# Performance work log

Hardware: AMD Instinct MI355X
Metric: run time of the kernel (lower is better)

## Reference

```python
import jax, jax.numpy as jnp
import numpy as np

ALPHA = 0.2  # LeakyReLU negative slope
NEG_INF = -9e15


def setup_inputs() -> dict:
    key = jax.random.key(0)
    ks = jax.random.split(key, 6)
    B, N, F_IN, F_OUT = 4, 1024, 64, 64
    h = jax.random.normal(ks[0], (B, N, F_IN), dtype=jnp.float32)
    adj = jax.random.randint(ks[1], (B, N, N), 0, 2, dtype=jnp.int32)
    lin_w = jax.random.normal(ks[2], (F_OUT, F_IN), dtype=jnp.float32) * (1.0 / np.sqrt(F_IN))
    lin_b = jax.random.normal(ks[3], (F_OUT,), dtype=jnp.float32) * 0.02
    W_w = jax.random.normal(ks[4], (F_OUT, 2 * F_OUT), dtype=jnp.float32) * (1.0 / np.sqrt(2 * F_OUT))
    a = jax.random.normal(ks[5], (F_OUT, 1), dtype=jnp.float32) * (1.414 / np.sqrt(F_OUT))
    return {"h": h, "adj": adj, "lin_w": lin_w, "lin_b": lin_b, "W_w": W_w, "a": a}


def reference(h, adj, lin_w, lin_b, W_w, a):
    F_OUT = lin_w.shape[0]
    # h' = Linear(h): (B, N, F_OUT)
    hp = jnp.einsum('bni,oi->bno', h, lin_w) + lin_b
    # W @ concat(h_i, h_j) == h_i @ W1^T + h_j @ W2^T  (same math, no 2F concat)
    W1, W2 = W_w[:, :F_OUT], W_w[:, F_OUT:]
    u = jnp.einsum('bnf,of->bno', hp, W1)  # source/row term   (B, N, F_OUT)
    v = jnp.einsum('bnf,of->bno', hp, W2)  # target/col term   (B, N, F_OUT)
    s = u[:, :, None, :] + v[:, None, :, :]        # (B, N, N, F_OUT)
    s = jnp.where(s > 0, s, ALPHA * s)             # LeakyReLU
    e = jnp.einsum('bijf,f->bij', s, a[:, 0])      # (B, N, N)
    e = jnp.where(adj > 0, e, NEG_INF)
    attention = jax.nn.softmax(e, axis=2)
    h_prime = jnp.einsum('bij,bjf->bif', attention, hp)
    return jax.nn.elu(h_prime)
```

## Files before the change

### kernel.cpp

```cpp
#include <hip/hip_runtime.h>
#include <hip/hip_bf16.h>
#include <math.h>

constexpr int B = 4;
constexpr int N = 1024;
constexpr float NEGINF = -9000000000000000.0f;

__global__ __launch_bounds__(512) void gat_wk0(
    const float* __restrict__ lin_w, const float* __restrict__ lin_b,
    const float* __restrict__ W_w, float* __restrict__ Wu, float* __restrict__ Wv,
    float* __restrict__ bu, float* __restrict__ bv) {
  __shared__ float lw[64 * 68];
  __shared__ float ww[64 * 132];
  __shared__ float lb[64];
  const int tid = threadIdx.x;
  for (int idx = tid; idx < 4096; idx += 512)
    lw[(idx >> 6) * 68 + (idx & 63)] = lin_w[idx];
  for (int idx = tid; idx < 8192; idx += 512)
    ww[(idx >> 7) * 132 + (idx & 127)] = W_w[idx];
  if (tid < 64) lb[tid] = lin_b[tid];
  __syncthreads();

  const int f = tid >> 3, i0 = (tid & 7) << 3;
  float wua[8], wva[8];
#pragma unroll
  for (int r = 0; r < 8; ++r) { wua[r] = 0.f; wva[r] = 0.f; }
  float bup = 0.f, bvp = 0.f;
#pragma unroll 4
  for (int o = 0; o < 64; ++o) {
    const float w1 = ww[f * 132 + o];
    const float w2 = ww[f * 132 + 64 + o];
    const float4 A = *(const float4*)&lw[o * 68 + i0];
    const float4 Bv = *(const float4*)&lw[o * 68 + i0 + 4];
    const float lv[8] = {A.x, A.y, A.z, A.w, Bv.x, Bv.y, Bv.z, Bv.w};
#pragma unroll
    for (int r = 0; r < 8; ++r) {
      wua[r] = fmaf(w1, lv[r], wua[r]);
      wva[r] = fmaf(w2, lv[r], wva[r]);
    }
    bup = fmaf(w1, lb[o], bup);
    bvp = fmaf(w2, lb[o], bvp);
  }
  *(float4*)&Wu[f * 64 + i0] = make_float4(wua[0], wua[1], wua[2], wua[3]);
  *(float4*)&Wu[f * 64 + i0 + 4] = make_float4(wua[4], wua[5], wua[6], wua[7]);
  *(float4*)&Wv[f * 64 + i0] = make_float4(wva[0], wva[1], wva[2], wva[3]);
  *(float4*)&Wv[f * 64 + i0 + 4] = make_float4(wva[4], wva[5], wva[6], wva[7]);
  if ((tid & 7) == 0) { bu[f] = bup; bv[f] = bvp; }
}

__global__ __launch_bounds__(256) void gat_prep(
    const float* __restrict__ h, const float* __restrict__ lin_w,
    const float* __restrict__ lin_b, const float* __restrict__ a_g,
    const float* __restrict__ Wu, const float* __restrict__ Wv,
    const float* __restrict__ bu_g, const float* __restrict__ bv_g,
    float* __restrict__ hp, float* __restrict__ u_out, float* __restrict__ vT,
    float* __restrict__ au_out, float* __restrict__ av_out) {
  __shared__ float hs[64 * 34];
  __shared__ float wl[64 * 68];
  __shared__ float wu[64 * 68];
  __shared__ float wv[64 * 68];
  __shared__ float vt_s[64 * 33];
  __shared__ float ared[2][32 * 17];
  __shared__ float lb_s[64], bu_s[64], bv_s[64], a_s[64];

  const int b = blockIdx.x >> 5;
  const int n0 = (blockIdx.x & 31) << 5;
  const int tid = threadIdx.x;

  for (int idx = tid; idx < 2048; idx += 256) {
    const int r = idx >> 6, c = idx & 63;
    hs[c * 34 + r] = h[((b << 10) + n0 + r) * 64 + c];
  }
  for (int idx = tid; idx < 4096; idx += 256) {
    const int r = idx >> 6, c = idx & 63;
    wl[c * 68 + r] = lin_w[idx];
    wu[c * 68 + r] = Wu[idx];
    wv[c * 68 + r] = Wv[idx];
  }
  if (tid < 64) {
    lb_s[tid] = lin_b[tid]; bu_s[tid] = bu_g[tid];
    bv_s[tid] = bv_g[tid];  a_s[tid] = a_g[tid];
  }
  __syncthreads();

  const int tf = tid & 15, tn = tid >> 4;
  float ahp[2][4], aU[2][4], aV[2][4];
#pragma unroll
  for (int q = 0; q < 2; ++q)
#pragma unroll
    for (int r = 0; r < 4; ++r) {
      ahp[q][r] = lb_s[tf * 4 + r];
      aU[q][r] = bu_s[tf * 4 + r];
      aV[q][r] = bv_s[tf * 4 + r];
    }
#pragma unroll 4
  for (int k = 0; k < 64; ++k) {
    const float2 h2 = *(const float2*)&hs[k * 34 + tn * 2];
    const float hv[2] = {h2.x, h2.y};
    const float4 l4 = *(const float4*)&wl[k * 68 + tf * 4];
    const float4 u4 = *(const float4*)&wu[k * 68 + tf * 4];
    const float4 v4 = *(const float4*)&wv[k * 68 + tf * 4];
    const float lv[4] = {l4.x, l4.y, l4.z, l4.w};
    const float uv[4] = {u4.x, u4.y, u4.z, u4.w};
    const float vv[4] = {v4.x, v4.y, v4.z, v4.w};
#pragma unroll
    for (int q = 0; q < 2; ++q)
#pragma unroll
      for (int r = 0; r < 4; ++r) {
        ahp[q][r] = fmaf(hv[q], lv[r], ahp[q][r]);
        aU[q][r] = fmaf(hv[q], uv[r], aU[q][r]);
        aV[q][r] = fmaf(hv[q], vv[r], aV[q][r]);
      }
  }
#pragma unroll
  for (int q = 0; q < 2; ++q) {
    const int row = (b << 10) + n0 + tn * 2 + q;
    *(float4*)&hp[row * 64 + tf * 4] =
        make_float4(ahp[q][0], ahp[q][1], ahp[q][2], ahp[q][3]);
    *(float4*)&u_out[row * 64 + tf * 4] =
        make_float4(aU[q][0], aU[q][1], aU[q][2], aU[q][3]);
  }
  float aup[2] = {0.f, 0.f}, avp[2] = {0.f, 0.f};
#pragma unroll
  for (int q = 0; q < 2; ++q)
#pragma unroll
    for (int r = 0; r < 4; ++r) {
      vt_s[(tf * 4 + r) * 33 + tn * 2 + q] = aV[q][r];
      aup[q] = fmaf(a_s[tf * 4 + r], aU[q][r], aup[q]);
      avp[q] = fmaf(a_s[tf * 4 + r], aV[q][r], avp[q]);
    }
#pragma unroll
  for (int q = 0; q < 2; ++q) {
    ared[0][(tn * 2 + q) * 17 + tf] = aup[q];
    ared[1][(tn * 2 + q) * 17 + tf] = avp[q];
  }
  __syncthreads();
  for (int idx = tid; idx < 2048; idx += 256) {
    const int f = idx >> 5, n = idx & 31;
    vT[(((b << 6) + f) << 10) + n0 + n] = vt_s[f * 33 + n];
  }
  if (tid < 64) {
    const int which = tid >> 5, row = tid & 31;
    float s2 = 0.f;
#pragma unroll
    for (int t = 0; t < 16; ++t) s2 += ared[which][row * 17 + t];
    if (which == 0) au_out[(b << 10) + n0 + row] = s2;
    else av_out[(b << 10) + n0 + row] = s2;
  }
}

__global__ __launch_bounds__(256) void gat_attn(
    const float* __restrict__ u_g, const float* __restrict__ vT,
    const float* __restrict__ hp, const int* __restrict__ adj,
    const float* __restrict__ a_g, const float* __restrict__ au_g,
    const float* __restrict__ av_g, float* __restrict__ out) {
  __shared__ float p_s[2 * 1024 * 4];
  __shared__ float u_s[64 * 8];
  __shared__ float a_s[64];
  __shared__ float au_s[8];
  __shared__ float wred[4 * 8];
  __shared__ float wsum[4 * 8];
  __shared__ float rinv_s[8];

  const int b = blockIdx.x >> 7;
  const int i0 = (blockIdx.x & 127) << 3;
  const int tid = threadIdx.x;
  const int lane = tid & 63, w = tid >> 6;

  if (tid < 64) a_s[tid] = a_g[tid];
  if (tid < 8) au_s[tid] = au_g[(b << 10) + i0 + tid];
  for (int idx = tid; idx < 512; idx += 256) {
    const int i = idx >> 6, f = idx & 63;
    u_s[f * 8 + i] = u_g[((b << 10) + i0 + i) * 64 + f];
  }
  __syncthreads();

  float e[8][4];
#pragma unroll
  for (int i = 0; i < 8; ++i)
#pragma unroll
    for (int k = 0; k < 4; ++k) e[i][k] = 0.f;

  const float* vb = vT + ((b << 6) << 10);
#pragma unroll 2
  for (int f = 0; f < 64; ++f) {
    const float af = a_s[f];
    float vv[4];
#pragma unroll
    for (int k = 0; k < 4; ++k) vv[k] = vb[(f << 10) + tid + (k << 8)];
    const float4 ua = *(const float4*)&u_s[f * 8];
    const float4 ub = *(const float4*)&u_s[f * 8 + 4];
    const float uu[8] = {ua.x, ua.y, ua.z, ua.w, ub.x, ub.y, ub.z, ub.w};
#pragma unroll
    for (int i = 0; i < 8; ++i)
#pragma unroll
      for (int k = 0; k < 4; ++k)
        e[i][k] = fmaf(af, fabsf(uu[i] + vv[k]), e[i][k]);
  }
  float avv[4];
#pragma unroll
  for (int k = 0; k < 4; ++k)
    avv[k] = 0.6f * av_g[(b << 10) + tid + (k << 8)];
  float au6[8];
#pragma unroll
  for (int i = 0; i < 8; ++i) au6[i] = 0.6f * au_s[i];
  const int* adjb = adj + ((((b << 10) + i0)) << 10) + tid;
#pragma unroll
  for (int i = 0; i < 8; ++i)
#pragma unroll
    for (int k = 0; k < 4; ++k) {
      const float ev = fmaf(0.4f, e[i][k], au6[i] + avv[k]);
      e[i][k] = adjb[(i << 10) + (k << 8)] > 0 ? ev : NEGINF;
    }

#pragma unroll
  for (int i = 0; i < 8; ++i) {
    float mm = fmaxf(fmaxf(e[i][0], e[i][1]), fmaxf(e[i][2], e[i][3]));
#pragma unroll
    for (int off = 32; off; off >>= 1) mm = fmaxf(mm, __shfl_xor(mm, off));
    if (lane == 0) wred[w * 8 + i] = mm;
  }
  __syncthreads();
#pragma unroll
  for (int i = 0; i < 8; ++i) {
    const float mi = fmaxf(fmaxf(wred[i], wred[8 + i]),
                           fmaxf(wred[16 + i], wred[24 + i]));
#pragma unroll
    for (int k = 0; k < 4; ++k) e[i][k] = __expf(e[i][k] - mi);
    float ss = e[i][0] + e[i][1] + e[i][2] + e[i][3];
#pragma unroll
    for (int off = 32; off; off >>= 1) ss += __shfl_xor(ss, off);
    if (lane == 0) wsum[w * 8 + i] = ss;
  }
  __syncthreads();
#pragma unroll
  for (int i = 0; i < 8; ++i) {
    const float stot = wsum[i] + wsum[8 + i] + wsum[16 + i] + wsum[24 + i];
    if (tid == i) rinv_s[i] = 1.0f / stot;
  }
#pragma unroll
  for (int k = 0; k < 4; ++k) {
    const int j = tid + (k << 8);
    *(float4*)&p_s[j << 2] = make_float4(e[0][k], e[1][k], e[2][k], e[3][k]);
    *(float4*)&p_s[4096 + (j << 2)] =
        make_float4(e[4][k], e[5][k], e[6][k], e[7][k]);
  }
  __syncthreads();

  const int fl = tid & 63, g = tid >> 6;
  float acc[8];
#pragma unroll
  for (int i = 0; i < 8; ++i) acc[i] = 0.f;
  const float* hpb = hp + (b << 16);
#pragma unroll 4
  for (int jj = g << 8; jj < (g << 8) + 256; ++jj) {
    const float hv = hpb[(jj << 6) + fl];
    const float4 p0 = *(const float4*)&p_s[jj << 2];
    const float4 p1 = *(const float4*)&p_s[4096 + (jj << 2)];
    acc[0] = fmaf(p0.x, hv, acc[0]);
    acc[1] = fmaf(p0.y, hv, acc[1]);
    acc[2] = fmaf(p0.z, hv, acc[2]);
    acc[3] = fmaf(p0.w, hv, acc[3]);
    acc[4] = fmaf(p1.x, hv, acc[4]);
    acc[5] = fmaf(p1.y, hv, acc[5]);
    acc[6] = fmaf(p1.z, hv, acc[6]);
    acc[7] = fmaf(p1.w, hv, acc[7]);
  }
  __syncthreads();
  float* red = p_s;
#pragma unroll
  for (int i = 0; i < 8; ++i) red[((g << 3) + i) << 6 | fl] = acc[i];
  __syncthreads();
#pragma unroll
  for (int o = 0; o < 2; ++o) {
    const int idx = tid + (o << 8);
    const int i = idx >> 6, f = idx & 63;
    float r = red[(i << 6) + f] + red[((8 + i) << 6) + f] +
              red[((16 + i) << 6) + f] + red[((24 + i) << 6) + f];
    r *= rinv_s[i];
    out[((b << 10) + i0 + i) * 64 + f] = r > 0.f ? r : expm1f(r);
  }
}

extern "C" void kernel_launch(void* const* d_in, const int* in_sizes, int n_in,
                              void* d_out, int out_size, void* d_ws, size_t ws_size,
                              hipStream_t stream) {
  const float* h = (const float*)d_in[0];
  const int* adj = (const int*)d_in[1];
  const float* lin_w = (const float*)d_in[2];
  const float* lin_b = (const float*)d_in[3];
  const float* W_w = (const float*)d_in[4];
  const float* a = (const float*)d_in[5];
  float* outp = (float*)d_out;

  float* ws = (float*)d_ws;
  float* hp = ws;
  float* u = ws + 262144;
  float* vT = ws + 524288;
  float* au = ws + 786432;
  float* av = ws + 790528;
  float* Wu = ws + 794624;
  float* Wv = ws + 798720;
  float* bu = ws + 802816;
  float* bv = ws + 802880;

  gat_wk0<<<dim3(1), dim3(512), 0, stream>>>(lin_w, lin_b, W_w, Wu, Wv, bu, bv);
  gat_prep<<<dim3(128), dim3(256), 0, stream>>>(h, lin_w, lin_b, a, Wu, Wv, bu,
                                                bv, hp, u, vT, au, av);
  gat_attn<<<dim3(512), dim3(256), 0, stream>>>(u, vT, hp, adj, a, au, av, outp);
}
```

Measured before the change: 135.6 us.

## Drop weight-fold kernel and halve attention rows per block with vectorized loads

Removes the single-block gat_wk0 launch that pre-multiplied W1/W2 by lin_w. gat_prep now computes hp first, stages it transposed in shared memory, and applies W1/W2 in a second pass. The attention kernel now handles 4 rows per block instead of 8, doubling the grid to 1024 blocks. It also gives each thread 4 contiguous columns so vT, av and adj can be read with float4/int4 loads. The extra blocks recompute the vT loads more often and add more duplicated reads of hp, in exchange for more parallelism, one fewer launch and wider memory accesses.

```diff
diff --git a/kernel.cpp b/kernel.cpp
--- a/kernel.cpp
+++ b/kernel.cpp
@@ -6,62 +6,20 @@
 constexpr int N = 1024;
 constexpr float NEGINF = -9000000000000000.0f;
 
-__global__ __launch_bounds__(512) void gat_wk0(
-    const float* __restrict__ lin_w, const float* __restrict__ lin_b,
-    const float* __restrict__ W_w, float* __restrict__ Wu, float* __restrict__ Wv,
-    float* __restrict__ bu, float* __restrict__ bv) {
-  __shared__ float lw[64 * 68];
-  __shared__ float ww[64 * 132];
-  __shared__ float lb[64];
-  const int tid = threadIdx.x;
-  for (int idx = tid; idx < 4096; idx += 512)
-    lw[(idx >> 6) * 68 + (idx & 63)] = lin_w[idx];
-  for (int idx = tid; idx < 8192; idx += 512)
-    ww[(idx >> 7) * 132 + (idx & 127)] = W_w[idx];
-  if (tid < 64) lb[tid] = lin_b[tid];
-  __syncthreads();
-
-  const int f = tid >> 3, i0 = (tid & 7) << 3;
-  float wua[8], wva[8];
-#pragma unroll
-  for (int r = 0; r < 8; ++r) { wua[r] = 0.f; wva[r] = 0.f; }
-  float bup = 0.f, bvp = 0.f;
-#pragma unroll 4
-  for (int o = 0; o < 64; ++o) {
-    const float w1 = ww[f * 132 + o];
-    const float w2 = ww[f * 132 + 64 + o];
-    const float4 A = *(const float4*)&lw[o * 68 + i0];
-    const float4 Bv = *(const float4*)&lw[o * 68 + i0 + 4];
-    const float lv[8] = {A.x, A.y, A.z, A.w, Bv.x, Bv.y, Bv.z, Bv.w};
-#pragma unroll
-    for (int r = 0; r < 8; ++r) {
-      wua[r] = fmaf(w1, lv[r], wua[r]);
-      wva[r] = fmaf(w2, lv[r], wva[r]);
-    }
-    bup = fmaf(w1, lb[o], bup);
-    bvp = fmaf(w2, lb[o], bvp);
-  }
-  *(float4*)&Wu[f * 64 + i0] = make_float4(wua[0], wua[1], wua[2], wua[3]);
-  *(float4*)&Wu[f * 64 + i0 + 4] = make_float4(wua[4], wua[5], wua[6], wua[7]);
-  *(float4*)&Wv[f * 64 + i0] = make_float4(wva[0], wva[1], wva[2], wva[3]);
-  *(float4*)&Wv[f * 64 + i0 + 4] = make_float4(wva[4], wva[5], wva[6], wva[7]);
-  if ((tid & 7) == 0) { bu[f] = bup; bv[f] = bvp; }
-}
-
 __global__ __launch_bounds__(256) void gat_prep(
     const float* __restrict__ h, const float* __restrict__ lin_w,
-    const float* __restrict__ lin_b, const float* __restrict__ a_g,
-    const float* __restrict__ Wu, const float* __restrict__ Wv,
-    const float* __restrict__ bu_g, const float* __restrict__ bv_g,
+    const float* __restrict__ lin_b, const float* __restrict__ W_w,
+    const float* __restrict__ a_g,
     float* __restrict__ hp, float* __restrict__ u_out, float* __restrict__ vT,
     float* __restrict__ au_out, float* __restrict__ av_out) {
   __shared__ float hs[64 * 34];
   __shared__ float wl[64 * 68];
-  __shared__ float wu[64 * 68];
-  __shared__ float wv[64 * 68];
+  __shared__ float w1[64 * 68];
+  __shared__ float w2[64 * 68];
+  __shared__ float hpT[64 * 34];
   __shared__ float vt_s[64 * 33];
   __shared__ float ared[2][32 * 17];
-  __shared__ float lb_s[64], bu_s[64], bv_s[64], a_s[64];
+  __shared__ float lb_s[64], a_s[64];
 
   const int b = blockIdx.x >> 5;
   const int n0 = (blockIdx.x & 31) << 5;
@@ -72,51 +30,61 @@
     hs[c * 34 + r] = h[((b << 10) + n0 + r) * 64 + c];
   }
   for (int idx = tid; idx < 4096; idx += 256) {
-    const int r = idx >> 6, c = idx & 63;
-    wl[c * 68 + r] = lin_w[idx];
-    wu[c * 68 + r] = Wu[idx];
-    wv[c * 68 + r] = Wv[idx];
-  }
-  if (tid < 64) {
-    lb_s[tid] = lin_b[tid]; bu_s[tid] = bu_g[tid];
-    bv_s[tid] = bv_g[tid];  a_s[tid] = a_g[tid];
-  }
+    const int o = idx >> 6, f = idx & 63;
+    wl[f * 68 + o] = lin_w[idx];
+    w1[f * 68 + o] = W_w[o * 128 + f];
+    w2[f * 68 + o] = W_w[o * 128 + 64 + f];
+  }
+  if (tid < 64) { lb_s[tid] = lin_b[tid]; a_s[tid] = a_g[tid]; }
   __syncthreads();
 
   const int tf = tid & 15, tn = tid >> 4;
-  float ahp[2][4], aU[2][4], aV[2][4];
+  float ahp[2][4];
 #pragma unroll
   for (int q = 0; q < 2; ++q)
 #pragma unroll
-    for (int r = 0; r < 4; ++r) {
-      ahp[q][r] = lb_s[tf * 4 + r];
-      aU[q][r] = bu_s[tf * 4 + r];
-      aV[q][r] = bv_s[tf * 4 + r];
-    }
+    for (int r = 0; r < 4; ++r) ahp[q][r] = lb_s[tf * 4 + r];
 #pragma unroll 4
   for (int k = 0; k < 64; ++k) {
     const float2 h2 = *(const float2*)&hs[k * 34 + tn * 2];
+    const float4 l4 = *(const float4*)&wl[k * 68 + tf * 4];
     const float hv[2] = {h2.x, h2.y};
-    const float4 l4 = *(const float4*)&wl[k * 68 + tf * 4];
-    const float4 u4 = *(const float4*)&wu[k * 68 + tf * 4];
-    const float4 v4 = *(const float4*)&wv[k * 68 + tf * 4];
     const float lv[4] = {l4.x, l4.y, l4.z, l4.w};
-    const float uv[4] = {u4.x, u4.y, u4.z, u4.w};
-    const float vv[4] = {v4.x, v4.y, v4.z, v4.w};
 #pragma unroll
     for (int q = 0; q < 2; ++q)
 #pragma unroll
-      for (int r = 0; r < 4; ++r) {
-        ahp[q][r] = fmaf(hv[q], lv[r], ahp[q][r]);
-        aU[q][r] = fmaf(hv[q], uv[r], aU[q][r]);
-        aV[q][r] = fmaf(hv[q], vv[r], aV[q][r]);
-      }
+      for (int r = 0; r < 4; ++r) ahp[q][r] = fmaf(hv[q], lv[r], ahp[q][r]);
   }
 #pragma unroll
   for (int q = 0; q < 2; ++q) {
     const int row = (b << 10) + n0 + tn * 2 + q;
     *(float4*)&hp[row * 64 + tf * 4] =
         make_float4(ahp[q][0], ahp[q][1], ahp[q][2], ahp[q][3]);
+#pragma unroll
+    for (int r = 0; r < 4; ++r) hpT[(tf * 4 + r) * 34 + tn * 2 + q] = ahp[q][r];
+  }
+  __syncthreads();
+
+  float aU[2][4] = {}, aV[2][4] = {};
+#pragma unroll 4
+  for (int k = 0; k < 64; ++k) {
+    const float2 h2 = *(const float2*)&hpT[k * 34 + tn * 2];
+    const float4 u4 = *(const float4*)&w1[k * 68 + tf * 4];
+    const float4 v4 = *(const float4*)&w2[k * 68 + tf * 4];
+    const float hv[2] = {h2.x, h2.y};
+    const float uv[4] = {u4.x, u4.y, u4.z, u4.w};
+    const float vv[4] = {v4.x, v4.y, v4.z, v4.w};
+#pragma unroll
+    for (int q = 0; q < 2; ++q)
+#pragma unroll
+      for (int r = 0; r < 4; ++r) {
+        aU[q][r] = fmaf(hv[q], uv[r], aU[q][r]);
+        aV[q][r] = fmaf(hv[q], vv[r], aV[q][r]);
+      }
+  }
+#pragma unroll
+  for (int q = 0; q < 2; ++q) {
+    const int row = (b << 10) + n0 + tn * 2 + q;
     *(float4*)&u_out[row * 64 + tf * 4] =
         make_float4(aU[q][0], aU[q][1], aU[q][2], aU[q][3]);
   }
@@ -154,129 +122,117 @@
     const float* __restrict__ hp, const int* __restrict__ adj,
     const float* __restrict__ a_g, const float* __restrict__ au_g,
     const float* __restrict__ av_g, float* __restrict__ out) {
-  __shared__ float p_s[2 * 1024 * 4];
-  __shared__ float u_s[64 * 8];
+  __shared__ float p_s[4 * 1024];
+  __shared__ float u_s[64 * 4];
   __shared__ float a_s[64];
-  __shared__ float au_s[8];
-  __shared__ float wred[4 * 8];
-  __shared__ float wsum[4 * 8];
-  __shared__ float rinv_s[8];
-
-  const int b = blockIdx.x >> 7;
-  const int i0 = (blockIdx.x & 127) << 3;
+  __shared__ float au_s[4];
+  __shared__ float wred[4][4];
+  __shared__ float wsum[4][4];
+  __shared__ float rinv_s[4];
+
+  const int b = blockIdx.x >> 8;
+  const int i0 = (blockIdx.x & 255) << 2;
   const int tid = threadIdx.x;
   const int lane = tid & 63, w = tid >> 6;
+  const int j0 = tid << 2;
 
   if (tid < 64) a_s[tid] = a_g[tid];
-  if (tid < 8) au_s[tid] = au_g[(b << 10) + i0 + tid];
-  for (int idx = tid; idx < 512; idx += 256) {
-    const int i = idx >> 6, f = idx & 63;
-    u_s[f * 8 + i] = u_g[((b << 10) + i0 + i) * 64 + f];
-  }
-  __syncthreads();
-
-  float e[8][4];
-#pragma unroll
-  for (int i = 0; i < 8; ++i)
+  if (tid < 4) au_s[tid] = au_g[(b << 10) + i0 + tid];
+  {
+    const int i = tid >> 6, f = tid & 63;
+    u_s[f * 4 + i] = u_g[((b << 10) + i0 + i) * 64 + f];
+  }
+  __syncthreads();
+
+  float e[4][4];
+#pragma unroll
+  for (int i = 0; i < 4; ++i)
 #pragma unroll
     for (int k = 0; k < 4; ++k) e[i][k] = 0.f;
 
   const float* vb = vT + ((b << 6) << 10);
-#pragma unroll 2
+#pragma unroll 4
   for (int f = 0; f < 64; ++f) {
     const float af = a_s[f];
-    float vv[4];
-#pragma unroll
-    for (int k = 0; k < 4; ++k) vv[k] = vb[(f << 10) + tid + (k << 8)];
-    const float4 ua = *(const float4*)&u_s[f * 8];
-    const float4 ub = *(const float4*)&u_s[f * 8 + 4];
-    const float uu[8] = {ua.x, ua.y, ua.z, ua.w, ub.x, ub.y, ub.z, ub.w};
-#pragma unroll
-    for (int i = 0; i < 8; ++i)
+    const float4 v4 = *(const float4*)&vb[(f << 10) + j0];
+    const float4 u4 = *(const float4*)&u_s[f * 4];
+    const float uu[4] = {u4.x, u4.y, u4.z, u4.w};
+    const float vv[4] = {v4.x, v4.y, v4.z, v4.w};
+#pragma unroll
+    for (int i = 0; i < 4; ++i)
 #pragma unroll
       for (int k = 0; k < 4; ++k)
         e[i][k] = fmaf(af, fabsf(uu[i] + vv[k]), e[i][k]);
   }
-  float avv[4];
-#pragma unroll
-  for (int k = 0; k < 4; ++k)
-    avv[k] = 0.6f * av_g[(b << 10) + tid + (k << 8)];
-  float au6[8];
-#pragma unroll
-  for (int i = 0; i < 8; ++i) au6[i] = 0.6f * au_s[i];
-  const int* adjb = adj + ((((b << 10) + i0)) << 10) + tid;
-#pragma unroll
-  for (int i = 0; i < 8; ++i)
+  const float4 av4 = *(const float4*)&av_g[(b << 10) + j0];
+  const float avv[4] = {0.6f * av4.x, 0.6f * av4.y, 0.6f * av4.z, 0.6f * av4.w};
+  float au6[4];
+#pragma unroll
+  for (int i = 0; i < 4; ++i) au6[i] = 0.6f * au_s[i];
+  const int* adjb = adj + ((((b << 10) + i0)) << 10) + j0;
+#pragma unroll
+  for (int i = 0; i < 4; ++i) {
+    const int4 ad = *(const int4*)&adjb[i << 10];
+    const int adv[4] = {ad.x, ad.y, ad.z, ad.w};
 #pragma unroll
     for (int k = 0; k < 4; ++k) {
       const float ev = fmaf(0.4f, e[i][k], au6[i] + avv[k]);
-      e[i][k] = adjb[(i << 10) + (k << 8)] > 0 ? ev : NEGINF;
+      e[i][k] = adv[k] > 0 ? ev : NEGINF;
     }
-
-#pragma unroll
-  for (int i = 0; i < 8; ++i) {
+  }
+
+#pragma unroll
+  for (int i = 0; i < 4; ++i) {
     float mm = fmaxf(fmaxf(e[i][0], e[i][1]), fmaxf(e[i][2], e[i][3]));
 #pragma unroll
     for (int off = 32; off; off >>= 1) mm = fmaxf(mm, __shfl_xor(mm, off));
-    if (lane == 0) wred[w * 8 + i] = mm;
-  }
-  __syncthreads();
-#pragma unroll
-  for (int i = 0; i < 8; ++i) {
-    const float mi = fmaxf(fmaxf(wred[i], wred[8 + i]),
-                           fmaxf(wred[16 + i], wred[24 + i]));
+    if (lane == 0) wred[w][i] = mm;
+  }
+  __syncthreads();
+#pragma unroll
+  for (int i = 0; i < 4; ++i) {
+    const float mi = fmaxf(fmaxf(wred[0][i], wred[1][i]),
+                           fmaxf(wred[2][i], wred[3][i]));
 #pragma unroll
     for (int k = 0; k < 4; ++k) e[i][k] = __expf(e[i][k] - mi);
     float ss = e[i][0] + e[i][1] + e[i][2] + e[i][3];
 #pragma unroll
     for (int off = 32; off; off >>= 1) ss += __shfl_xor(ss, off);
-    if (lane == 0) wsum[w * 8 + i] = ss;
-  }
-  __syncthreads();
-#pragma unroll
-  for (int i = 0; i < 8; ++i) {
-    const float stot = wsum[i] + wsum[8 + i] + wsum[16 + i] + wsum[24 + i];
-    if (tid == i) rinv_s[i] = 1.0f / stot;
-  }
-#pragma unroll
-  for (int k = 0; k < 4; ++k) {
-    const int j = tid + (k << 8);
-    *(float4*)&p_s[j << 2] = make_float4(e[0][k], e[1][k], e[2][k], e[3][k]);
-    *(float4*)&p_s[4096 + (j << 2)] =
-        make_float4(e[4][k], e[5][k], e[6][k], e[7][k]);
-  }
+    if (lane == 0) wsum[w][i] = ss;
+  }
+  __syncthreads();
+  if (tid < 4)
+    rinv_s[tid] = 1.0f / (wsum[0][tid] + wsum[1][tid] + wsum[2][tid] + wsum[3][tid]);
+#pragma unroll
+  for (int i = 0; i < 4; ++i)
+    *(float4*)&p_s[(i << 10) + j0] = make_float4(e[i][0], e[i][1], e[i][2], e[i][3]);
   __syncthreads();
 
   const int fl = tid & 63, g = tid >> 6;
-  float acc[8];
-#pragma unroll
-  for (int i = 0; i < 8; ++i) acc[i] = 0.f;
+  float acc[4] = {0.f, 0.f, 0.f, 0.f};
   const float* hpb = hp + (b << 16);
-#pragma unroll 4
-  for (int jj = g << 8; jj < (g << 8) + 256; ++jj) {
-    const float hv = hpb[(jj << 6) + fl];
-    const float4 p0 = *(const float4*)&p_s[jj << 2];
-    const float4 p1 = *(const float4*)&p_s[4096 + (jj << 2)];
-    acc[0] = fmaf(p0.x, hv, acc[0]);
-    acc[1] = fmaf(p0.y, hv, acc[1]);
-    acc[2] = fmaf(p0.z, hv, acc[2]);
-    acc[3] = fmaf(p0.w, hv, acc[3]);
-    acc[4] = fmaf(p1.x, hv, acc[4]);
-    acc[5] = fmaf(p1.y, hv, acc[5]);
-    acc[6] = fmaf(p1.z, hv, acc[6]);
-    acc[7] = fmaf(p1.w, hv, acc[7]);
+  for (int jj = g << 8; jj < (g << 8) + 256; jj += 4) {
+    const float4 p0 = *(const float4*)&p_s[jj];
+    const float4 p1 = *(const float4*)&p_s[1024 + jj];
+    const float4 p2 = *(const float4*)&p_s[2048 + jj];
+    const float4 p3 = *(const float4*)&p_s[3072 + jj];
+    float hv[4];
+#pragma unroll
+    for (int t = 0; t < 4; ++t) hv[t] = hpb[((jj + t) << 6) + fl];
+    acc[0] += p0.x * hv[0] + p0.y * hv[1] + p0.z * hv[2] + p0.w * hv[3];
+    acc[1] += p1.x * hv[0] + p1.y * hv[1] + p1.z * hv[2] + p1.w * hv[3];
+    acc[2] += p2.x * hv[0] + p2.y * hv[1] + p2.z * hv[2] + p2.w * hv[3];
+    acc[3] += p3.x * hv[0] + p3.y * hv[1] + p3.z * hv[2] + p3.w * hv[3];
   }
   __syncthreads();
   float* red = p_s;
 #pragma unroll
-  for (int i = 0; i < 8; ++i) red[((g << 3) + i) << 6 | fl] = acc[i];
-  __syncthreads();
-#pragma unroll
-  for (int o = 0; o < 2; ++o) {
-    const int idx = tid + (o << 8);
-    const int i = idx >> 6, f = idx & 63;
-    float r = red[(i << 6) + f] + red[((8 + i) << 6) + f] +
-              red[((16 + i) << 6) + f] + red[((24 + i) << 6) + f];
+  for (int i = 0; i < 4; ++i) red[(((g << 2) + i) << 6) + fl] = acc[i];
+  __syncthreads();
+  {
+    const int i = tid >> 6, f = tid & 63;
+    float r = red[((i) << 6) + f] + red[((4 + i) << 6) + f] +
+              red[((8 + i) << 6) + f] + red[((12 + i) << 6) + f];
     r *= rinv_s[i];
     out[((b << 10) + i0 + i) * 64 + f] = r > 0.f ? r : expm1f(r);
   }
@@ -299,13 +255,8 @@
   float* vT = ws + 524288;
   float* au = ws + 786432;
   float* av = ws + 790528;
-  float* Wu = ws + 794624;
-  float* Wv = ws + 798720;
-  float* bu = ws + 802816;
-  float* bv = ws + 802880;
-
-  gat_wk0<<<dim3(1), dim3(512), 0, stream>>>(lin_w, lin_b, W_w, Wu, Wv, bu, bv);
-  gat_prep<<<dim3(128), dim3(256), 0, stream>>>(h, lin_w, lin_b, a, Wu, Wv, bu,
-                                                bv, hp, u, vT, au, av);
-  gat_attn<<<dim3(512), dim3(256), 0, stream>>>(u, vT, hp, adj, a, au, av, outp);
+
+  gat_prep<<<dim3(128), dim3(256), 0, stream>>>(h, lin_w, lin_b, W_w, a,
+                                                hp, u, vT, au, av);
+  gat_attn<<<dim3(1024), dim3(256), 0, stream>>>(u, vT, hp, adj, a, au, av, outp);
 }
```

Result: faster. 119.3 us (-12.0%).
